# Kernel optimization log

Hardware: AMD Instinct MI355X
Metric: run time of the kernel (lower is better)

## Reference

```python
import jax, jax.numpy as jnp
import numpy as np

EMBED_DIM = 1024
HEAD_DIM = 64


def setup_inputs() -> dict:
    key = jax.random.key(0)
    k1, k2, k3, k4 = jax.random.split(key, 4)
    B, T = 4, 4096
    x = jax.random.normal(k1, (B, T, EMBED_DIM), dtype=jnp.float32)
    # nn.Linear(EMBED_DIM, head_dim, bias=False): store as (EMBED_DIM, head_dim)
    s = (1.0 / np.sqrt(EMBED_DIM)).astype(np.float32)
    Wk = jax.random.uniform(k2, (EMBED_DIM, HEAD_DIM), jnp.float32, -s, s)
    Wq = jax.random.uniform(k3, (EMBED_DIM, HEAD_DIM), jnp.float32, -s, s)
    Wv = jax.random.uniform(k4, (EMBED_DIM, HEAD_DIM), jnp.float32, -s, s)
    return {"x": x, "Wq": Wq, "Wk": Wk, "Wv": Wv}


def reference(x, Wq, Wk, Wv):
    B, T, E = x.shape
    q = jnp.einsum('bte,ed->btd', x, Wq)  # (B,T,D)
    k = jnp.einsum('bte,ed->btd', x, Wk)
    v = jnp.einsum('bte,ed->btd', x, Wv)
    # NOTE: original scales by EMBED_DIM**-0.5 (x.size(-1)), not head_dim**-0.5
    scale = jnp.asarray(E, x.dtype) ** -0.5
    scores = jnp.einsum('bqd,bkd->bqk', q, k) * scale  # (B,T,T)
    causal = jnp.tril(jnp.ones((T, T), dtype=bool))
    scores = jnp.where(causal, scores, jnp.asarray(-jnp.inf, scores.dtype))
    attn = jax.nn.softmax(scores, axis=-1)
    # dropout is identity at inference (deterministic baseline)
    out = jnp.einsum('bqk,bkd->bqd', attn, v)  # (B,T,D)
    return out
```

## Files before the change

kernel.cpp:

```cpp
#include <hip/hip_runtime.h>
#include <hip/hip_bf16.h>
#include <stdint.h>

#define BATCH 4
#define SEQ   4096
#define EMB   1024
#define HD    64

typedef __bf16 bf16x8 __attribute__((ext_vector_type(8)));
typedef float  f32x4  __attribute__((ext_vector_type(4)));
typedef unsigned short u16;

union ABFrag { u16 s[8]; bf16x8 v; };

__device__ __forceinline__ u16 f2bf_rne(float f) {
    union { float f; uint32_t u; } cv; cv.f = f;
    uint32_t u = cv.u;
    return (u16)((u + 0x7fffu + ((u >> 16) & 1u)) >> 16);
}
__device__ __forceinline__ float bf2f(u16 h) {
    union { uint32_t u; float f; } cv; cv.u = ((uint32_t)h) << 16;
    return cv.f;
}
__device__ __forceinline__ void gld16(const void* g, void* l) {
    __builtin_amdgcn_global_load_lds(
        (const __attribute__((address_space(1))) void*)g,
        (__attribute__((address_space(3))) void*)l, 16, 0, 0);
}

__global__ __launch_bounds__(256) void wt_kernel(
        const float* __restrict__ Wq, const float* __restrict__ Wk,
        const float* __restrict__ Wv, u16* __restrict__ Wt) {
    int idx = blockIdx.x * 256 + threadIdx.x;
    int i = idx >> 16;
    int r = idx & 65535;
    int n = r >> 10;
    int k = r & 1023;
    const float* W = (i == 0) ? Wq : (i == 1) ? Wk : Wv;
    Wt[idx] = f2bf_rne(W[k * HD + n]);
}

__global__ __launch_bounds__(256) void qkv_kernel(
        const float* __restrict__ x, const u16* __restrict__ Wt,
        u16* __restrict__ Qw, u16* __restrict__ Kw, u16* __restrict__ Vt) {
    __shared__ float xs[2][2048];
    __shared__ u16   wsb[2][12288];

    const int t    = threadIdx.x;
    const int wave = t >> 6;
    const int lane = t & 63;
    const int m16  = lane & 15;
    const int quad = lane >> 4;
    const int rh   = wave & 1;
    const int ch   = wave >> 1;
    const int R0   = blockIdx.x * 32;

    #define ISSUE(buf_, kt_) do {                                              \
        const int r4_ = lane >> 4, c16_ = lane & 15;                           \
        _Pragma("unroll")                                                      \
        for (int j_ = 0; j_ < 2; ++j_) {                                       \
            const int ii_  = wave + (j_ << 2);                                 \
            const int row_ = (ii_ << 2) + r4_;                      \
            const int kc_  = c16_ ^ (row_ & 15);                               \
            gld16(x + (size_t)(R0 + row_) * EMB + ((kt_) << 6) + (kc_ << 2),   \
                  &xs[buf_][ii_ << 8]);                                        \
        }                                                                      \
        const int r8_ = lane >> 3, c8_ = lane & 7;                             \
        _Pragma("unroll")                                                      \
        for (int j_ = 0; j_ < 6; ++j_) {                                       \
            const int rb_ = (wave * 6 + j_) << 3;                  \
            const int kw_ = c8_ ^ r8_;                                         \
            gld16(Wt + (size_t)(rb_ + r8_) * 1024 + ((kt_) << 6) + (kw_ << 3), \
                  &wsb[buf_][(wave * 6 + j_) << 9]);                           \
        }                                                                      \
    } while (0)

    f32x4 acc[6];
#pragma unroll
    for (int a = 0; a < 6; ++a) acc[a] = (f32x4){0.f, 0.f, 0.f, 0.f};

    const int row_x = rh * 16 + m16;
    ISSUE(0, 0);

    for (int kt = 0; kt < 16; ++kt) {
        const int buf = kt & 1;
        __syncthreads();
        if (kt < 15) ISSUE(buf ^ 1, kt + 1);

#pragma unroll
        for (int ks2 = 0; ks2 < 2; ++ks2) {
            const int c0 = (ks2 << 3) + (quad << 1);
            const float4 a0 = *(const float4*)&xs[buf][(row_x << 6) + ((c0 ^ m16) << 2)];
            const float4 a1 = *(const float4*)&xs[buf][(row_x << 6) + (((c0 + 1) ^ m16) << 2)];
            ABFrag af;
            af.s[0] = f2bf_rne(a0.x); af.s[1] = f2bf_rne(a0.y);
            af.s[2] = f2bf_rne(a0.z); af.s[3] = f2bf_rne(a0.w);
            af.s[4] = f2bf_rne(a1.x); af.s[5] = f2bf_rne(a1.y);
            af.s[6] = f2bf_rne(a1.z); af.s[7] = f2bf_rne(a1.w);
#pragma unroll
            for (int i = 0; i < 6; ++i) {
                const int tt   = ch * 6 + i;
                const int rowW = (tt << 4) + m16;
                const bf16x8 bf = *(const bf16x8*)&wsb[buf][
                        (rowW << 6) + ((((ks2 << 2) + quad) ^ (m16 & 7)) << 3)];
                acc[i] = __builtin_amdgcn_mfma_f32_16x16x32_bf16(af.v, bf, acc[i], 0, 0, 0);
            }
        }
    }
    #undef ISSUE

    const int rowbase = R0 + rh * 16 + (quad << 2);
    const int bidx = rowbase >> 12;
    const int t0   = rowbase & 4095;
#pragma unroll
    for (int i = 0; i < 6; ++i) {
        const int tt  = ch * 6 + i;
        const int w3  = tt >> 2;
        const int col = ((tt & 3) << 4) + m16;
        if (w3 == 0) {
#pragma unroll
            for (int reg = 0; reg < 4; ++reg)
                Qw[(size_t)(rowbase + reg) * HD + col] = f2bf_rne(acc[i][reg] * 0.03125f);
        } else if (w3 == 1) {
#pragma unroll
            for (int reg = 0; reg < 4; ++reg)
                Kw[(size_t)(rowbase + reg) * HD + col] = f2bf_rne(acc[i][reg]);
        } else {
            ushort4 vv;
            vv.x = f2bf_rne(acc[i][0]); vv.y = f2bf_rne(acc[i][1]);
            vv.z = f2bf_rne(acc[i][2]); vv.w = f2bf_rne(acc[i][3]);
            *(ushort4*)(Vt + (size_t)((bidx << 6) + col) * SEQ + t0) = vv;
        }
    }
}

__global__ __launch_bounds__(256) void attn_part_kernel(
        const u16* __restrict__ Qw, const u16* __restrict__ Kw,
        const u16* __restrict__ Vt, u16* __restrict__ Opart,
        float* __restrict__ Mp, float* __restrict__ Lp) {
    __shared__ u16 kv[2][2][4096];
    __shared__ u16 ldsP[4][16 * 72];

    const int pid = blockIdx.x;
    const int r   = pid >> 8;
    const int i   = pid & 255;
    const int b   = i & 3;
    const int h   = i >> 2;
    const int qt  = h ^ (int)((0x1f203f00u >> (r * 8)) & 63u);
    const int c   = r;
    const int p_out = (((b << 6) + qt) << 2) + c;

    const int wave = threadIdx.x >> 6;
    const int lane = threadIdx.x & 63;
    const int m16  = lane & 15;
    const int quad = lane >> 4;

    #define ISSUE_KV(buf_, jt_) do {                                           \
        const int r8_ = lane >> 3, c8_ = lane & 7;                             \
        const int kc_ = c8_ ^ r8_;                                             \
        _Pragma("unroll")                                                      \
        for (int j_ = 0; j_ < 2; ++j_) {                                       \
            const int row_ = ((wave * 2 + j_) << 3) + r8_;          \
            gld16(Kw + ((size_t)(b * SEQ + ((jt_) << 6) + row_) << 6) + (kc_ << 3), \
                  &kv[buf_][0][(wave * 2 + j_) << 9]);                         \
            gld16(Vt + (size_t)((b << 6) + row_) * SEQ + ((jt_) << 6) + (kc_ << 3), \
                  &kv[buf_][1][(wave * 2 + j_) << 9]);                         \
        }                                                                      \
    } while (0)

    const int qrow = (qt << 6) + (wave << 4) + m16;
    const u16* qbase = Qw + ((size_t)(b * SEQ + qrow) << 6);
    const bf16x8 qf0 = *(const bf16x8*)(qbase + (quad << 3));
    const bf16x8 qf1 = *(const bf16x8*)(qbase + 32 + (quad << 3));

    f32x4 acc[4];
#pragma unroll
    for (int dt = 0; dt < 4; ++dt) acc[dt] = (f32x4){0.f, 0.f, 0.f, 0.f};
    float m_i = -3.0e38f;
    float l_i = 0.f;

    u16* ldsW = &ldsP[wave][0];
    const int xs0 = (quad ^ (m16 & 7)) << 3;
    const int xs1 = (((quad + 4)) ^ (m16 & 7)) << 3;

    if (c <= qt) ISSUE_KV(0, c);

    int buf = 0;
    for (int jt = c; jt <= qt; jt += 4) {
        __syncthreads();
        if (jt + 4 <= qt) ISSUE_KV(buf ^ 1, jt + 4);

        f32x4 s[4];
#pragma unroll
        for (int mt = 0; mt < 4; ++mt) {
            const int base = ((mt << 4) + m16) << 6;
            bf16x8 k0 = *(const bf16x8*)&kv[buf][0][base + xs0];
            bf16x8 k1 = *(const bf16x8*)&kv[buf][0][base + xs1];
            s[mt] = (f32x4){0.f, 0.f, 0.f, 0.f};
            s[mt] = __builtin_amdgcn_mfma_f32_16x16x32_bf16(k0, qf0, s[mt], 0, 0, 0);
            s[mt] = __builtin_amdgcn_mfma_f32_16x16x32_bf16(k1, qf1, s[mt], 0, 0, 0);
        }

        if (jt == qt) {
            const int q_in = (wave << 4) + m16;
#pragma unroll
            for (int mt = 0; mt < 4; ++mt) {
                const int k_in = (mt << 4) + (quad << 2);
#pragma unroll
                for (int reg = 0; reg < 4; ++reg)
                    if (k_in + reg > q_in) s[mt][reg] = -3.0e38f;
            }
        }

        float tm = fmaxf(fmaxf(s[0][0], s[0][1]), fmaxf(s[0][2], s[0][3]));
#pragma unroll
        for (int mt = 1; mt < 4; ++mt)
            tm = fmaxf(tm, fmaxf(fmaxf(s[mt][0], s[mt][1]), fmaxf(s[mt][2], s[mt][3])));
        tm = fmaxf(tm, __shfl_xor(tm, 16));
        tm = fmaxf(tm, __shfl_xor(tm, 32));

        const float mnew  = fmaxf(m_i, tm);
        const float alpha = __expf(m_i - mnew);
        m_i = mnew;

        float psum = 0.f;
#pragma unroll
        for (int mt = 0; mt < 4; ++mt) {
            const float p0 = __expf(s[mt][0] - mnew);
            const float p1 = __expf(s[mt][1] - mnew);
            const float p2 = __expf(s[mt][2] - mnew);
            const float p3 = __expf(s[mt][3] - mnew);
            psum += (p0 + p1) + (p2 + p3);
            ushort4 pv;
            pv.x = f2bf_rne(p0); pv.y = f2bf_rne(p1);
            pv.z = f2bf_rne(p2); pv.w = f2bf_rne(p3);
            *(ushort4*)(ldsW + m16 * 72 + (mt << 4) + (quad << 2)) = pv;
        }
        l_i = l_i * alpha + psum;
#pragma unroll
        for (int dt = 0; dt < 4; ++dt)
#pragma unroll
            for (int reg = 0; reg < 4; ++reg) acc[dt][reg] *= alpha;

        const bf16x8 p0 = *(const bf16x8*)(ldsW + m16 * 72 + (quad << 3));
        const bf16x8 p1 = *(const bf16x8*)(ldsW + m16 * 72 + 32 + (quad << 3));
#pragma unroll
        for (int dt = 0; dt < 4; ++dt) {
            const int base = ((dt << 4) + m16) << 6;
            bf16x8 v0 = *(const bf16x8*)&kv[buf][1][base + xs0];
            bf16x8 v1 = *(const bf16x8*)&kv[buf][1][base + xs1];
            acc[dt] = __builtin_amdgcn_mfma_f32_16x16x32_bf16(v0, p0, acc[dt], 0, 0, 0);
            acc[dt] = __builtin_amdgcn_mfma_f32_16x16x32_bf16(v1, p1, acc[dt], 0, 0, 0);
        }
        buf ^= 1;
    }
    #undef ISSUE_KV

    float l = l_i;
    l += __shfl_xor(l, 16);
    l += __shfl_xor(l, 32);

    u16* ob = Opart + (size_t)p_out * 4096;
    const int qin = (wave << 4) + m16;
#pragma unroll
    for (int dt = 0; dt < 4; ++dt) {
        ushort4 vv;
        vv.x = f2bf_rne(acc[dt][0]); vv.y = f2bf_rne(acc[dt][1]);
        vv.z = f2bf_rne(acc[dt][2]); vv.w = f2bf_rne(acc[dt][3]);
        *(ushort4*)(ob + qin * 64 + (dt << 4) + (quad << 2)) = vv;
    }
    if (quad == 0) {
        Mp[p_out * 64 + qin] = m_i;
        Lp[p_out * 64 + qin] = l;
    }
}

__global__ __launch_bounds__(256) void combine_kernel(
        const u16* __restrict__ Opart, const float* __restrict__ Mp,
        const float* __restrict__ Lp, float* __restrict__ out) {
    __shared__ float sm[4][16];
    __shared__ float sl[4][16];
    const int bq = blockIdx.x >> 2;
    const int rq = blockIdx.x & 3;
    const int pidbase = bq << 2;
    const int t = threadIdx.x;
    if (t < 64) {
        const int cc = t >> 4, rr = t & 15;
        sm[cc][rr] = Mp[(pidbase + cc) * 64 + rq * 16 + rr];
        sl[cc][rr] = Lp[(pidbase + cc) * 64 + rq * 16 + rr];
    }
    __syncthreads();

    const int row_l = t >> 4;
    const int c4    = (t & 15) << 2;
    const int row   = rq * 16 + row_l;

    const float M = fmaxf(fmaxf(sm[0][row_l], sm[1][row_l]),
                          fmaxf(sm[2][row_l], sm[3][row_l]));
    float n0 = 0.f, n1 = 0.f, n2 = 0.f, n3 = 0.f, den = 0.f;
#pragma unroll
    for (int cc = 0; cc < 4; ++cc) {
        const float w = __expf(sm[cc][row_l] - M);
        den += w * sl[cc][row_l];
        const ushort4 op = *(const ushort4*)&Opart[
                (size_t)(pidbase + cc) * 4096 + row * 64 + c4];
        n0 += w * bf2f(op.x); n1 += w * bf2f(op.y);
        n2 += w * bf2f(op.z); n3 += w * bf2f(op.w);
    }
    const float rd = 1.0f / den;
    float4 o; o.x = n0 * rd; o.y = n1 * rd; o.z = n2 * rd; o.w = n3 * rd;
    *(float4*)&out[((size_t)bq << 12) + (row << 6) + c4] = o;
}

extern "C" void kernel_launch(void* const* d_in, const int* in_sizes, int n_in,
                              void* d_out, int out_size, void* d_ws, size_t ws_size,
                              hipStream_t stream) {
    const float* x  = (const float*)d_in[0];
    const float* Wq = (const float*)d_in[1];
    const float* Wk = (const float*)d_in[2];
    const float* Wv = (const float*)d_in[3];
    float* out = (float*)d_out;

    char* ws = (char*)d_ws;
    u16* Qw    = (u16*)(ws);
    u16* Kw    = (u16*)(ws + (2u << 20));
    u16* Vt    = (u16*)(ws + (4u << 20));
    u16* Wt    = (u16*)(ws + (6u << 20));
    u16* Opart = (u16*)(ws + (13u << 19));
    float* Mp  = (float*)(ws + (29u << 19));
    float* Lp  = (float*)(ws + (59u << 18));

    wt_kernel<<<768, 256, 0, stream>>>(Wq, Wk, Wv, Wt);
    qkv_kernel<<<512, 256, 0, stream>>>(x, Wt, Qw, Kw, Vt);
    attn_part_kernel<<<1024, 256, 0, stream>>>(Qw, Kw, Vt, Opart, Mp, Lp);
    combine_kernel<<<1024, 256, 0, stream>>>(Opart, Mp, Lp, out);
}
```

Before: 147.5 us.

## Use exp2 with log2e-folded Q scale, lazy rescaling, native bf16 casts, swizzled P LDS

The log2(e) factor is folded into the Q scale so that every softmax and combine exponential becomes a raw exp2 instruction. The online-softmax rescale of the accumulator and running sum now happens only when the tile max exceeds the running max by more than a threshold, tested wave-uniformly with __any. Hand-written RNE bf16 conversion is replaced with native __bf16 casts, the per-wave P scratch buffer uses an XOR-swizzled layout instead of padding, and attn_part_kernel gets an occupancy hint. Lazy rescaling lets exponentials reach up to 2^8 before renormalisation, which adds some bf16 precision risk in P.

```diff
diff --git a/kernel.cpp b/kernel.cpp
--- a/kernel.cpp
+++ b/kernel.cpp
@@ -11,12 +11,10 @@
 typedef float  f32x4  __attribute__((ext_vector_type(4)));
 typedef unsigned short u16;
 
-union ABFrag { u16 s[8]; bf16x8 v; };
-
-__device__ __forceinline__ u16 f2bf_rne(float f) {
-    union { float f; uint32_t u; } cv; cv.f = f;
-    uint32_t u = cv.u;
-    return (u16)((u + 0x7fffu + ((u >> 16) & 1u)) >> 16);
+#define QSCALE 0.04508422002777948f
+
+__device__ __forceinline__ u16 f2bf(float f) {
+    union { __bf16 h; u16 u; } c; c.h = (__bf16)f; return c.u;
 }
 __device__ __forceinline__ float bf2f(u16 h) {
     union { uint32_t u; float f; } cv; cv.u = ((uint32_t)h) << 16;
@@ -37,7 +35,7 @@
     int n = r >> 10;
     int k = r & 1023;
     const float* W = (i == 0) ? Wq : (i == 1) ? Wk : Wv;
-    Wt[idx] = f2bf_rne(W[k * HD + n]);
+    Wt[idx] = f2bf(W[k * HD + n]);
 }
 
 __global__ __launch_bounds__(256) void qkv_kernel(
@@ -92,11 +90,11 @@
             const int c0 = (ks2 << 3) + (quad << 1);
             const float4 a0 = *(const float4*)&xs[buf][(row_x << 6) + ((c0 ^ m16) << 2)];
             const float4 a1 = *(const float4*)&xs[buf][(row_x << 6) + (((c0 + 1) ^ m16) << 2)];
-            ABFrag af;
-            af.s[0] = f2bf_rne(a0.x); af.s[1] = f2bf_rne(a0.y);
-            af.s[2] = f2bf_rne(a0.z); af.s[3] = f2bf_rne(a0.w);
-            af.s[4] = f2bf_rne(a1.x); af.s[5] = f2bf_rne(a1.y);
-            af.s[6] = f2bf_rne(a1.z); af.s[7] = f2bf_rne(a1.w);
+            union { bf16x8 v; __bf16 e[8]; } af;
+            af.e[0] = (__bf16)a0.x; af.e[1] = (__bf16)a0.y;
+            af.e[2] = (__bf16)a0.z; af.e[3] = (__bf16)a0.w;
+            af.e[4] = (__bf16)a1.x; af.e[5] = (__bf16)a1.y;
+            af.e[6] = (__bf16)a1.z; af.e[7] = (__bf16)a1.w;
 #pragma unroll
             for (int i = 0; i < 6; ++i) {
                 const int tt   = ch * 6 + i;
@@ -120,26 +118,26 @@
         if (w3 == 0) {
 #pragma unroll
             for (int reg = 0; reg < 4; ++reg)
-                Qw[(size_t)(rowbase + reg) * HD + col] = f2bf_rne(acc[i][reg] * 0.03125f);
+                Qw[(size_t)(rowbase + reg) * HD + col] = f2bf(acc[i][reg] * QSCALE);
         } else if (w3 == 1) {
 #pragma unroll
             for (int reg = 0; reg < 4; ++reg)
-                Kw[(size_t)(rowbase + reg) * HD + col] = f2bf_rne(acc[i][reg]);
+                Kw[(size_t)(rowbase + reg) * HD + col] = f2bf(acc[i][reg]);
         } else {
-            ushort4 vv;
-            vv.x = f2bf_rne(acc[i][0]); vv.y = f2bf_rne(acc[i][1]);
-            vv.z = f2bf_rne(acc[i][2]); vv.w = f2bf_rne(acc[i][3]);
-            *(ushort4*)(Vt + (size_t)((bidx << 6) + col) * SEQ + t0) = vv;
-        }
-    }
-}
-
-__global__ __launch_bounds__(256) void attn_part_kernel(
+            union { ushort4 vv; __bf16 e[4]; } o;
+            o.e[0] = (__bf16)acc[i][0]; o.e[1] = (__bf16)acc[i][1];
+            o.e[2] = (__bf16)acc[i][2]; o.e[3] = (__bf16)acc[i][3];
+            *(ushort4*)(Vt + (size_t)((bidx << 6) + col) * SEQ + t0) = o.vv;
+        }
+    }
+}
+
+__global__ __launch_bounds__(256, 4) void attn_part_kernel(
         const u16* __restrict__ Qw, const u16* __restrict__ Kw,
         const u16* __restrict__ Vt, u16* __restrict__ Opart,
         float* __restrict__ Mp, float* __restrict__ Lp) {
     __shared__ u16 kv[2][2][4096];
-    __shared__ u16 ldsP[4][16 * 72];
+    __shared__ u16 ldsP[4][1024];
 
     const int pid = blockIdx.x;
     const int r   = pid >> 8;
@@ -182,6 +180,7 @@
     u16* ldsW = &ldsP[wave][0];
     const int xs0 = (quad ^ (m16 & 7)) << 3;
     const int xs1 = (((quad + 4)) ^ (m16 & 7)) << 3;
+    const int psw = m16 & 7;
 
     if (c <= qt) ISSUE_KV(0, c);
 
@@ -219,31 +218,35 @@
         tm = fmaxf(tm, __shfl_xor(tm, 16));
         tm = fmaxf(tm, __shfl_xor(tm, 32));
 
-        const float mnew  = fmaxf(m_i, tm);
-        const float alpha = __expf(m_i - mnew);
-        m_i = mnew;
+        if (__any(tm > m_i + 8.0f)) {
+            const float mnew  = fmaxf(m_i, tm);
+            const float alpha = __builtin_amdgcn_exp2f(m_i - mnew);
+            m_i = mnew;
+            l_i *= alpha;
+#pragma unroll
+            for (int dt = 0; dt < 4; ++dt)
+#pragma unroll
+                for (int reg = 0; reg < 4; ++reg) acc[dt][reg] *= alpha;
+        }
 
         float psum = 0.f;
 #pragma unroll
         for (int mt = 0; mt < 4; ++mt) {
-            const float p0 = __expf(s[mt][0] - mnew);
-            const float p1 = __expf(s[mt][1] - mnew);
-            const float p2 = __expf(s[mt][2] - mnew);
-            const float p3 = __expf(s[mt][3] - mnew);
+            const float p0 = __builtin_amdgcn_exp2f(s[mt][0] - m_i);
+            const float p1 = __builtin_amdgcn_exp2f(s[mt][1] - m_i);
+            const float p2 = __builtin_amdgcn_exp2f(s[mt][2] - m_i);
+            const float p3 = __builtin_amdgcn_exp2f(s[mt][3] - m_i);
             psum += (p0 + p1) + (p2 + p3);
-            ushort4 pv;
-            pv.x = f2bf_rne(p0); pv.y = f2bf_rne(p1);
-            pv.z = f2bf_rne(p2); pv.w = f2bf_rne(p3);
-            *(ushort4*)(ldsW + m16 * 72 + (mt << 4) + (quad << 2)) = pv;
-        }
-        l_i = l_i * alpha + psum;
-#pragma unroll
-        for (int dt = 0; dt < 4; ++dt)
-#pragma unroll
-            for (int reg = 0; reg < 4; ++reg) acc[dt][reg] *= alpha;
-
-        const bf16x8 p0 = *(const bf16x8*)(ldsW + m16 * 72 + (quad << 3));
-        const bf16x8 p1 = *(const bf16x8*)(ldsW + m16 * 72 + 32 + (quad << 3));
+            union { ushort4 pv; __bf16 e[4]; } u;
+            u.e[0] = (__bf16)p0; u.e[1] = (__bf16)p1;
+            u.e[2] = (__bf16)p2; u.e[3] = (__bf16)p3;
+            const int c8 = ((mt << 1) + (quad >> 1)) ^ psw;
+            *(ushort4*)(ldsW + (m16 << 6) + (c8 << 3) + ((quad & 1) << 2)) = u.pv;
+        }
+        l_i += psum;
+
+        const bf16x8 p0 = *(const bf16x8*)(ldsW + (m16 << 6) + ((quad ^ psw) << 3));
+        const bf16x8 p1 = *(const bf16x8*)(ldsW + (m16 << 6) + (((quad + 4) ^ psw) << 3));
 #pragma unroll
         for (int dt = 0; dt < 4; ++dt) {
             const int base = ((dt << 4) + m16) << 6;
@@ -264,10 +267,10 @@
     const int qin = (wave << 4) + m16;
 #pragma unroll
     for (int dt = 0; dt < 4; ++dt) {
-        ushort4 vv;
-        vv.x = f2bf_rne(acc[dt][0]); vv.y = f2bf_rne(acc[dt][1]);
-        vv.z = f2bf_rne(acc[dt][2]); vv.w = f2bf_rne(acc[dt][3]);
-        *(ushort4*)(ob + qin * 64 + (dt << 4) + (quad << 2)) = vv;
+        union { ushort4 vv; __bf16 e[4]; } o;
+        o.e[0] = (__bf16)acc[dt][0]; o.e[1] = (__bf16)acc[dt][1];
+        o.e[2] = (__bf16)acc[dt][2]; o.e[3] = (__bf16)acc[dt][3];
+        *(ushort4*)(ob + qin * 64 + (dt << 4) + (quad << 2)) = o.vv;
     }
     if (quad == 0) {
         Mp[p_out * 64 + qin] = m_i;
@@ -300,7 +303,7 @@
     float n0 = 0.f, n1 = 0.f, n2 = 0.f, n3 = 0.f, den = 0.f;
 #pragma unroll
     for (int cc = 0; cc < 4; ++cc) {
-        const float w = __expf(sm[cc][row_l] - M);
+        const float w = __builtin_amdgcn_exp2f(sm[cc][row_l] - M);
         den += w * sl[cc][row_l];
         const ushort4 op = *(const ushort4*)&Opart[
                 (size_t)(pidbase + cc) * 4096 + row * 64 + c4];
```

Result: faster. 144.4 us (-2.1%).
